# Kernel tuning notes

Measured on AMD Instinct MI355X. Metric: run time of the kernel, lower is better.

## Reference

```python
import jax, jax.numpy as jnp
import numpy as np

B, T, E, H = 2, 2048, 1024, 16


def setup_inputs() -> dict:
    key = jax.random.key(0)
    ks = jax.random.split(key, 8)
    # VarianceScaling(1.0) ~ truncated normal with stddev ~ sqrt(1/fan_in)
    std = 1.0 / np.sqrt(E)
    x = jax.random.normal(ks[0], (B, T, E), dtype=jnp.float32)
    y = jax.random.normal(ks[1], (B, T, E), dtype=jnp.float32)
    # causal mask [1, 1, T, T]
    mask = jnp.tril(jnp.ones((T, T), dtype=jnp.float32))[None, None]
    Wq = jax.random.normal(ks[2], (E, E), dtype=jnp.float32) * std
    Wk = jax.random.normal(ks[3], (E, E), dtype=jnp.float32) * std
    Wv = jax.random.normal(ks[4], (E, E), dtype=jnp.float32) * std
    Wo = jax.random.normal(ks[5], (E, E), dtype=jnp.float32) * std
    bq = jnp.zeros((E,), jnp.float32)
    bk = jnp.zeros((E,), jnp.float32)
    bv = jnp.zeros((E,), jnp.float32)
    bo = jnp.zeros((E,), jnp.float32)
    return {"x": x, "y": y, "mask": mask, "Wq": Wq, "bq": bq,
            "Wk": Wk, "bk": bk, "Wv": Wv, "bv": bv, "Wo": Wo, "bo": bo,
            "num_heads": H}


def reference(x, y, mask, Wq, bq, Wk, bk, Wv, bv, Wo, bo, num_heads):
    Bx, Tq, Emb = x.shape
    Tkv = y.shape[1]
    d = Emb // num_heads
    q = (x @ Wq + bq).reshape(Bx, Tq, num_heads, d)
    k = (y @ Wk + bk).reshape(Bx, Tkv, num_heads, d)
    v = (y @ Wv + bv).reshape(Bx, Tkv, num_heads, d)
    scale = 1.0 / np.sqrt(d).astype(np.float32)
    att = scale * jnp.einsum('bthd,bThd->bhtT', q, k)  # [B,H,Tq,Tkv]
    att = att * mask - 1e10 * (1.0 - mask)
    att = jax.nn.softmax(att, axis=-1)
    out = jnp.einsum('bhtT,bThd->bthd', att, v).reshape(Bx, Tq, Emb)
    return out @ Wo + bo
```

## Files before the change

### kernel.cpp

```cpp
#include <hip/hip_runtime.h>
#include <stdint.h>

#define BB 2
#define TT 2048
#define EE 1024
#define HH 16
#define DD 64
#define MM (BB*TT)

typedef unsigned short u16;
typedef __attribute__((ext_vector_type(4))) float f32x4;
typedef __attribute__((ext_vector_type(8))) __bf16 bf16x8;
typedef __attribute__((ext_vector_type(8))) u16 u16x8;
typedef __attribute__((ext_vector_type(4))) u16 u16x4;

union FragU { u16x8 u; bf16x8 b; };
union BfU { __bf16 h; u16 u; };

__device__ __forceinline__ u16 f2bf(float f) {
  uint32_t u = __float_as_uint(f);
  u += 0x7fffu + ((u >> 16) & 1u);
  return (u16)(u >> 16);
}

__device__ __forceinline__ void gload16(const u16* __restrict__ g, u16* l) {
  __builtin_amdgcn_global_load_lds((const __attribute__((address_space(1))) void*)g,
                                   (__attribute__((address_space(3))) void*)l, 16, 0, 0);
}

__global__ __launch_bounds__(256) void prep(const float* __restrict__ x, const float* __restrict__ y,
                                            const float* __restrict__ Wq, const float* __restrict__ Wk,
                                            const float* __restrict__ Wv, const float* __restrict__ Wo,
                                            u16* __restrict__ xb, u16* __restrict__ yb,
                                            u16* __restrict__ Wqt, u16* __restrict__ Wkvt,
                                            u16* __restrict__ Wot) {
  __shared__ alignas(16) float tile[64][65];
  int bi = blockIdx.x, t = threadIdx.x;
  if (bi < 4096) {
    const float* src = (bi < 2048) ? x : y;
    u16* dst = (bi < 2048) ? xb : yb;
    int i = (bi & 2047) * 256 + t;
    const f32x4* s4 = (const f32x4*)src;
    f32x4 a = s4[2*i], b = s4[2*i+1];
    u16x8 o;
    o[0]=f2bf(a[0]); o[1]=f2bf(a[1]); o[2]=f2bf(a[2]); o[3]=f2bf(a[3]);
    o[4]=f2bf(b[0]); o[5]=f2bf(b[1]); o[6]=f2bf(b[2]); o[7]=f2bf(b[3]);
    ((u16x8*)dst)[i] = o;
    return;
  }
  int wi = bi - 4096;
  int z = wi >> 8;
  const float* W; u16* Tp;
  switch (z) {
    case 0: W = Wq; Tp = Wqt; break;
    case 1: W = Wk; Tp = Wkvt; break;
    case 2: W = Wv; Tp = Wkvt + (size_t)1024*EE; break;
    default: W = Wo; Tp = Wot; break;
  }
  int r8 = wi & 255;
  int n0 = (r8 & 15) * 64, k0 = (r8 >> 4) * 64;
#pragma unroll
  for (int i = 0; i < 16; ++i) {
    int idx = i*256 + t; int r = idx >> 6, c = idx & 63;
    tile[r][c] = W[(size_t)(k0 + r) * EE + n0 + c];
  }
  __syncthreads();
#pragma unroll
  for (int i = 0; i < 16; ++i) {
    int idx = i*256 + t; int rn = idx >> 6, ck = idx & 63;
    Tp[(size_t)(n0 + rn) * EE + k0 + ck] = f2bf(tile[ck][rn]);
  }
}

template <int BM, int EPI>
__device__ __forceinline__ void gemm_body(const u16* __restrict__ A, const u16* __restrict__ Bt,
                                          const float* __restrict__ bias, void* __restrict__ Cout,
                                          int N, int K, float oscale, int bm, int bn,
                                          u16 (*As)[64], u16 (*Bs)[64]) {
  constexpr int MI = BM / 32;
  const int t = threadIdx.x;
  const int lane = t & 63, w = t >> 6;
  const int wr = w >> 1, wc = w & 1;
  const int g = lane >> 4, cl = lane & 15;

  f32x4 acc[MI][4] = {};

  const u16* Ag = A + (size_t)(bm * BM) * K;
  const u16* Bg = Bt + (size_t)(bn * 128) * K;

  const int rl = lane >> 3;
  const int sw = ((lane & 7) ^ rl) * 8;

  const int nk = K / 64;
  for (int kt = 0; kt < nk; ++kt) {
    const int k0 = kt * 64;
    __syncthreads();
#pragma unroll
    for (int j = 0; j < MI; ++j) {
      int ca = w * MI + j;
      gload16(Ag + (size_t)(ca*8 + rl) * K + k0 + sw, &As[ca*8][0]);
    }
#pragma unroll
    for (int j = 0; j < 4; ++j) {
      int cb = w * 4 + j;
      gload16(Bg + (size_t)(cb*8 + rl) * K + k0 + sw, &Bs[cb*8][0]);
    }
    __syncthreads();
#pragma unroll
    for (int ks = 0; ks < 2; ++ks) {
      FragU af[MI], bfr[4];
#pragma unroll
      for (int mi = 0; mi < MI; ++mi) {
        int row = wr*(BM/2) + mi*16 + cl;
        af[mi].u = *(const u16x8*)&As[row][((ks*4 + g) ^ (row & 7)) * 8];
      }
#pragma unroll
      for (int nj = 0; nj < 4; ++nj) {
        int row = wc*64 + nj*16 + cl;
        bfr[nj].u = *(const u16x8*)&Bs[row][((ks*4 + g) ^ (row & 7)) * 8];
      }
#pragma unroll
      for (int mi = 0; mi < MI; ++mi)
#pragma unroll
        for (int nj = 0; nj < 4; ++nj)
          acc[mi][nj] = __builtin_amdgcn_mfma_f32_16x16x32_bf16(af[mi].b, bfr[nj].b, acc[mi][nj], 0, 0, 0);
    }
  }

  const int cbase = bn*128 + wc*64 + cl;
  float bv[4];
#pragma unroll
  for (int nj = 0; nj < 4; ++nj) bv[nj] = bias[cbase + nj*16];
#pragma unroll
  for (int mi = 0; mi < MI; ++mi) {
    int row0 = bm*BM + wr*(BM/2) + mi*16 + (g << 2);
    if (EPI == 2) {
      int bb = row0 >> 11;
      int tt = row0 & 2047;
      int tb64 = tt & ~63;
      int w6 = tt & 63;
      int p = ((w6 >> 5) << 5) | (((w6 >> 2) & 3) << 3) | (((w6 >> 4) & 1) << 2);
#pragma unroll
      for (int nj = 0; nj < 4; ++nj) {
        int cc = cbase + nj*16;
        int hh = cc >> 6, dd = cc & 63;
        u16x4 v;
#pragma unroll
        for (int i = 0; i < 4; ++i) v[i] = f2bf(acc[mi][nj][i] + bv[nj]);
        *(u16x4*)((u16*)Cout + ((size_t)((bb*HH + hh)*DD + dd))*2048 + tb64 + p) = v;
      }
    } else {
#pragma unroll
      for (int i = 0; i < 4; ++i) {
        if (EPI == 1) {
          float* Cp = (float*)Cout + (size_t)(row0 + i) * N + cbase;
#pragma unroll
          for (int nj = 0; nj < 4; ++nj)
            Cp[nj*16] = (acc[mi][nj][i] + bv[nj]) * oscale;
        } else {
          u16* Cp = (u16*)Cout + (size_t)(row0 + i) * N + cbase;
#pragma unroll
          for (int nj = 0; nj < 4; ++nj)
            Cp[nj*16] = f2bf((acc[mi][nj][i] + bv[nj]) * oscale);
        }
      }
    }
  }
}

__global__ __launch_bounds__(256) void gemm_qkv(const u16* __restrict__ xb, const u16* __restrict__ yb,
                                                const u16* __restrict__ Wqt, const u16* __restrict__ Wkvt,
                                                const float* __restrict__ bq, const float* __restrict__ bk,
                                                const float* __restrict__ bv,
                                                u16* __restrict__ Qb, u16* __restrict__ Kb,
                                                u16* __restrict__ Vtb, float c1) {
  __shared__ alignas(16) u16 As[128][64];
  __shared__ alignas(16) u16 Bs[128][64];
  const int i = blockIdx.x;
  const int l = (i & 7) * 96 + (i >> 3);
  const int bm = l / 24, bx = l % 24;
  if (bx < 8)
    gemm_body<128, 0>(xb, Wqt, bq, Qb, 1024, EE, c1, bm, bx, As, Bs);
  else if (bx < 16)
    gemm_body<128, 0>(yb, Wkvt, bk, Kb, 1024, EE, 1.0f, bm, bx - 8, As, Bs);
  else
    gemm_body<128, 2>(yb, Wkvt + (size_t)1024*EE, bv, Vtb, 1024, EE, 1.0f, bm, bx - 16, As, Bs);
}

__global__ __launch_bounds__(256) void gemm_o(const u16* __restrict__ Atb, const u16* __restrict__ Wot,
                                              const float* __restrict__ bo, float* __restrict__ out) {
  __shared__ alignas(16) u16 As[64][64];
  __shared__ alignas(16) u16 Bs[128][64];
  const int i = blockIdx.x;
  const int l = (i & 7) * 64 + (i >> 3);
  const int bm = l / 8, bn = l % 8;
  gemm_body<64, 1>(Atb, Wot, bo, out, 1024, EE, 1.0f, bm, bn, As, Bs);
}

__global__ __launch_bounds__(512, 4) void attn(const u16* __restrict__ Q, const u16* __restrict__ Kb,
                                               const u16* __restrict__ Vt, u16* __restrict__ O) {
  const int i0 = blockIdx.x;
  const int qq = i0 >> 8, a = (i0 >> 5) & 7, bh = i0 & 31;
  int qt;
  switch (qq) {
    case 0:  qt = 31 - a; break;
    case 1:  qt = 16 + a; break;
    case 2:  qt = 15 - a; break;
    default: qt = a;      break;
  }
  const int b = bh >> 4, h = bh & 15;

  const int t = threadIdx.x, lane = t & 63, w = t >> 6;
  const int ws_ = w & 3;
  const int hi = w >> 2;
  const int g = lane >> 4, c = lane & 15;
  __shared__ alignas(16) u16 Ks[2][64][72];
  __shared__ alignas(16) u16 Vs[2][64][72];

  const int qw0 = qt * 64 + ws_ * 16;

  FragU qf[2];
  const u16* Qbase = Q + ((size_t)(b*TT) + qw0) * EE + h*DD;
#pragma unroll
  for (int ks = 0; ks < 2; ++ks)
    qf[ks].u = *(const u16x8*)(Qbase + (size_t)c * EE + ks*32 + g*8);

  f32x4 oacc[4] = {};
  float l_part = 0.f;
  float m_run = -1e30f;

  const u16* Kbase = Kb + (size_t)(b*TT) * 1024 + h*DD;
  const u16* Vtbase = Vt + (size_t)(b*HH + h) * DD * 2048;

  const int nkv = qt + 1;
  const int npair = (nkv + 1) >> 1;

  const int srow = t >> 3;
  const int scol = (t & 7) * 8;

  u16x8 rk[2], rv[2];
  rk[0] = *(const u16x8*)(Kbase + (size_t)srow * 1024 + scol);
  rv[0] = *(const u16x8*)(Vtbase + (size_t)srow * 2048 + scol);
  if (1 < nkv) {
    rk[1] = *(const u16x8*)(Kbase + (size_t)(64 + srow) * 1024 + scol);
    rv[1] = *(const u16x8*)(Vtbase + (size_t)srow * 2048 + 64 + scol);
  }

  for (int jj = 0; jj < npair; ++jj) {
    const int j0 = 2*jj;
    __syncthreads();
    *(u16x8*)&Ks[0][srow][scol] = rk[0];
    *(u16x8*)&Vs[0][srow][scol] = rv[0];
    if (j0 + 1 < nkv) {
      *(u16x8*)&Ks[1][srow][scol] = rk[1];
      *(u16x8*)&Vs[1][srow][scol] = rv[1];
    }
    __syncthreads();
    if (jj + 1 < npair) {
      const int jn = 2*(jj + 1);
      rk[0] = *(const u16x8*)(Kbase + (size_t)(jn*64 + srow) * 1024 + scol);
      rv[0] = *(const u16x8*)(Vtbase + (size_t)srow * 2048 + jn*64 + scol);
      if (jn + 1 < nkv) {
        rk[1] = *(const u16x8*)(Kbase + (size_t)((jn+1)*64 + srow) * 1024 + scol);
        rv[1] = *(const u16x8*)(Vtbase + (size_t)srow * 2048 + (jn+1)*64 + scol);
      }
    }
    const int j = j0 + hi;
    const int kv0 = j * 64;
    if (j >= nkv || kv0 > qw0 + 15) continue;

    f32x4 s[4] = {};
    __builtin_amdgcn_s_setprio(1);
#pragma unroll
    for (int ks = 0; ks < 2; ++ks) {
      const int kc = ks*32 + g*8;
      FragU kf[4];
#pragma unroll
      for (int nj = 0; nj < 4; ++nj)
        kf[nj].u = *(const u16x8*)&Ks[hi][nj*16 + c][kc];
#pragma unroll
      for (int nj = 0; nj < 4; ++nj)
        s[nj] = __builtin_amdgcn_mfma_f32_16x16x32_bf16(kf[nj].b, qf[ks].b, s[nj], 0, 0, 0);
    }
    __builtin_amdgcn_s_setprio(0);

    const bool full = (kv0 + 63 <= qw0);
    float vmax;
    if (full) {
      float m0 = fmaxf(fmaxf(s[0][0], s[0][1]), fmaxf(s[0][2], s[0][3]));
      float m1 = fmaxf(fmaxf(s[1][0], s[1][1]), fmaxf(s[1][2], s[1][3]));
      float m2 = fmaxf(fmaxf(s[2][0], s[2][1]), fmaxf(s[2][2], s[2][3]));
      float m3 = fmaxf(fmaxf(s[3][0], s[3][1]), fmaxf(s[3][2], s[3][3]));
      vmax = fmaxf(fmaxf(m0, m1), fmaxf(m2, m3));
    } else {
      const int q = qw0 + c;
      vmax = -1e30f;
#pragma unroll
      for (int nj = 0; nj < 4; ++nj)
#pragma unroll
        for (int r = 0; r < 4; ++r) {
          float xv = s[nj][r];
          if (kv0 + nj*16 + 4*g + r > q) xv = -1e30f;
          s[nj][r] = xv;
          vmax = fmaxf(vmax, xv);
        }
    }

    if (__any(vmax > m_run + 8.f)) {
      float vm = vmax;
      vm = fmaxf(vm, __shfl_xor(vm, 1));
      vm = fmaxf(vm, __shfl_xor(vm, 2));
      vm = fmaxf(vm, __shfl_xor(vm, 4));
      vm = fmaxf(vm, __shfl_xor(vm, 8));
      vm = fmaxf(vm, __shfl_xor(vm, 16));
      vm = fmaxf(vm, __shfl_xor(vm, 32));
      float f = exp2f(m_run - vm);
      l_part *= f;
#pragma unroll
      for (int dj = 0; dj < 4; ++dj)
#pragma unroll
        for (int i = 0; i < 4; ++i) oacc[dj][i] *= f;
      m_run = vm;
    }

    FragU pa[2];
    float psum = 0.f;
#pragma unroll
    for (int nj = 0; nj < 4; ++nj)
#pragma unroll
      for (int r = 0; r < 4; ++r) {
        float p = exp2f(s[nj][r] - m_run);
        psum += p;
        BfU cv; cv.h = (__bf16)p;
        pa[nj >> 1].u[(nj & 1) * 4 + r] = cv.u;
      }
    l_part += psum;

    __builtin_amdgcn_s_setprio(1);
#pragma unroll
    for (int ks = 0; ks < 2; ++ks) {
#pragma unroll
      for (int dj = 0; dj < 4; ++dj) {
        FragU vf;
        vf.u = *(const u16x8*)&Vs[hi][dj*16 + c][ks*32 + g*8];
        oacc[dj] = __builtin_amdgcn_mfma_f32_16x16x32_bf16(pa[ks].b, vf.b, oacc[dj], 0, 0, 0);
      }
    }
    __builtin_amdgcn_s_setprio(0);
  }

  __syncthreads();
  l_part += __shfl_xor(l_part, 16);
  l_part += __shfl_xor(l_part, 32);

  float* mO = (float*)&Ks[0][0][0];
  float* mL = (float*)&Vs[0][0][0];

  if (hi) {
#pragma unroll
    for (int i = 0; i < 4; ++i) {
      int row = 4*g + i;
#pragma unroll
      for (int dj = 0; dj < 4; ++dj)
        mO[((size_t)(ws_*16 + row))*66 + dj*16 + c] = oacc[dj][i];
    }
    if (lane < 16) mL[ws_*16 + lane] = l_part;
    if (lane == 0) mL[64 + ws_] = m_run;
  }
  __syncthreads();
  if (!hi) {
    float m1 = mL[64 + ws_];
    float l1 = mL[ws_*16 + c];
    float mN = fmaxf(m_run, m1);
    float f0 = exp2f(m_run - mN);
    float f1 = exp2f(m1 - mN);
    float lm = l_part * f0 + l1 * f1;
    u16* Ob = O + ((size_t)(b*TT) + qw0) * EE + h*DD;
#pragma unroll
    for (int i = 0; i < 4; ++i) {
      int row = 4*g + i;
      float li = __shfl(lm, row);
      float inv = 1.f / li;
#pragma unroll
      for (int dj = 0; dj < 4; ++dj) {
        float o1 = mO[((size_t)(ws_*16 + row))*66 + dj*16 + c];
        Ob[(size_t)row * EE + dj*16 + c] = f2bf((oacc[dj][i] * f0 + o1 * f1) * inv);
      }
    }
  }
}

extern "C" void kernel_launch(void* const* d_in, const int* in_sizes, int n_in,
                              void* d_out, int out_size, void* d_ws, size_t ws_size,
                              hipStream_t stream) {
  const float* x  = (const float*)d_in[0];
  const float* y  = (const float*)d_in[1];
  const float* Wq = (const float*)d_in[3];
  const float* bq = (const float*)d_in[4];
  const float* Wk = (const float*)d_in[5];
  const float* bk = (const float*)d_in[6];
  const float* Wv = (const float*)d_in[7];
  const float* bv = (const float*)d_in[8];
  const float* Wo = (const float*)d_in[9];
  const float* bo = (const float*)d_in[10];

  if (ws_size < (size_t)58720256) return;

  char* ws = (char*)d_ws;
  u16* Wqt  = (u16*)(ws + 0);
  u16* Wkvt = (u16*)(ws + 2097152);
  u16* Wot  = (u16*)(ws + 6291456);
  u16* Qb   = (u16*)(ws + 8388608);
  u16* Kb   = (u16*)(ws + 16777216);
  u16* Vtb  = (u16*)(ws + 25165824);
  u16* Atb  = (u16*)(ws + 33554432);
  u16* xb   = (u16*)(ws + 41943040);
  u16* yb   = (u16*)(ws + 50331648);

  const float c1 = 0.125f * 1.44269504088896340736f;

  prep<<<5120, 256, 0, stream>>>(x, y, Wq, Wk, Wv, Wo, xb, yb, Wqt, Wkvt, Wot);
  gemm_qkv<<<768, 256, 0, stream>>>(xb, yb, Wqt, Wkvt, bq, bk, bv, Qb, Kb, Vtb, c1);
  attn<<<1024, 512, 0, stream>>>(Qb, Kb, Vtb, Atb);
  gemm_o<<<512, 256, 0, stream>>>(Atb, Wot, bo, (float*)d_out);
}
```

Before: 118.5 us.

## Split long causal attention tiles across blocks with separate merge kernel

Replaces the in-block two-wavegroup KV split with a split-KV scheme. Query tiles in the upper half of the sequence are split into two blocks that each cover half of the KV range and write unnormalized partial outputs and softmax stats to workspace. A new merge kernel combines the two partials. Shorter tiles run whole in 256-thread blocks. The aim is better load balance and occupancy, at the cost of an extra launch and fp32 partial traffic. The partial buffer reuses the xb/yb workspace region.

```diff
diff --git a/kernel.cpp b/kernel.cpp
--- a/kernel.cpp
+++ b/kernel.cpp
@@ -16,6 +16,8 @@
 
 union FragU { u16x8 u; bf16x8 b; };
 union BfU { __bf16 h; u16 u; };
+
+#define PSLOT 4224
 
 __device__ __forceinline__ u16 f2bf(float f) {
   uint32_t u = __float_as_uint(f);
@@ -197,27 +199,32 @@
   gemm_body<64, 1>(Atb, Wot, bo, out, 1024, EE, 1.0f, bm, bn, As, Bs);
 }
 
-__global__ __launch_bounds__(512, 4) void attn(const u16* __restrict__ Q, const u16* __restrict__ Kb,
-                                               const u16* __restrict__ Vt, u16* __restrict__ O) {
+__global__ __launch_bounds__(256, 6) void attn(const u16* __restrict__ Q, const u16* __restrict__ Kb,
+                                               const u16* __restrict__ Vt, u16* __restrict__ O,
+                                               float* __restrict__ Pp) {
   const int i0 = blockIdx.x;
-  const int qq = i0 >> 8, a = (i0 >> 5) & 7, bh = i0 & 31;
-  int qt;
-  switch (qq) {
-    case 0:  qt = 31 - a; break;
-    case 1:  qt = 16 + a; break;
-    case 2:  qt = 15 - a; break;
-    default: qt = a;      break;
+  const int bh = i0 & 31, u = i0 >> 5;
+  int qt, c0, c1;
+  bool partial;
+  if (u < 32) {
+    qt = 31 - (u >> 1);
+    const int nkv = qt + 1, mid = (nkv + 1) >> 1;
+    c0 = (u & 1) ? mid : 0;
+    c1 = (u & 1) ? nkv : mid;
+    partial = true;
+  } else {
+    qt = 47 - u;
+    c0 = 0; c1 = qt + 1;
+    partial = false;
   }
   const int b = bh >> 4, h = bh & 15;
 
   const int t = threadIdx.x, lane = t & 63, w = t >> 6;
-  const int ws_ = w & 3;
-  const int hi = w >> 2;
   const int g = lane >> 4, c = lane & 15;
-  __shared__ alignas(16) u16 Ks[2][64][72];
-  __shared__ alignas(16) u16 Vs[2][64][72];
-
-  const int qw0 = qt * 64 + ws_ * 16;
+  __shared__ alignas(16) u16 Ks[64][72];
+  __shared__ alignas(16) u16 Vs[64][72];
+
+  const int qw0 = qt * 64 + w * 16;
 
   FragU qf[2];
   const u16* Qbase = Q + ((size_t)(b*TT) + qw0) * EE + h*DD;
@@ -232,42 +239,34 @@
   const u16* Kbase = Kb + (size_t)(b*TT) * 1024 + h*DD;
   const u16* Vtbase = Vt + (size_t)(b*HH + h) * DD * 2048;
 
-  const int nkv = qt + 1;
-  const int npair = (nkv + 1) >> 1;
-
-  const int srow = t >> 3;
+  const int srow0 = t >> 3;
+  const int srow1 = 32 + srow0;
   const int scol = (t & 7) * 8;
 
   u16x8 rk[2], rv[2];
-  rk[0] = *(const u16x8*)(Kbase + (size_t)srow * 1024 + scol);
-  rv[0] = *(const u16x8*)(Vtbase + (size_t)srow * 2048 + scol);
-  if (1 < nkv) {
-    rk[1] = *(const u16x8*)(Kbase + (size_t)(64 + srow) * 1024 + scol);
-    rv[1] = *(const u16x8*)(Vtbase + (size_t)srow * 2048 + 64 + scol);
-  }
-
-  for (int jj = 0; jj < npair; ++jj) {
-    const int j0 = 2*jj;
+  {
+    const int kv0 = c0 * 64;
+    rk[0] = *(const u16x8*)(Kbase + (size_t)(kv0 + srow0) * 1024 + scol);
+    rk[1] = *(const u16x8*)(Kbase + (size_t)(kv0 + srow1) * 1024 + scol);
+    rv[0] = *(const u16x8*)(Vtbase + (size_t)srow0 * 2048 + kv0 + scol);
+    rv[1] = *(const u16x8*)(Vtbase + (size_t)srow1 * 2048 + kv0 + scol);
+  }
+
+  for (int j = c0; j < c1; ++j) {
+    const int kv0 = j * 64;
     __syncthreads();
-    *(u16x8*)&Ks[0][srow][scol] = rk[0];
-    *(u16x8*)&Vs[0][srow][scol] = rv[0];
-    if (j0 + 1 < nkv) {
-      *(u16x8*)&Ks[1][srow][scol] = rk[1];
-      *(u16x8*)&Vs[1][srow][scol] = rv[1];
-    }
+    *(u16x8*)&Ks[srow0][scol] = rk[0];
+    *(u16x8*)&Ks[srow1][scol] = rk[1];
+    *(u16x8*)&Vs[srow0][scol] = rv[0];
+    *(u16x8*)&Vs[srow1][scol] = rv[1];
     __syncthreads();
-    if (jj + 1 < npair) {
-      const int jn = 2*(jj + 1);
-      rk[0] = *(const u16x8*)(Kbase + (size_t)(jn*64 + srow) * 1024 + scol);
-      rv[0] = *(const u16x8*)(Vtbase + (size_t)srow * 2048 + jn*64 + scol);
-      if (jn + 1 < nkv) {
-        rk[1] = *(const u16x8*)(Kbase + (size_t)((jn+1)*64 + srow) * 1024 + scol);
-        rv[1] = *(const u16x8*)(Vtbase + (size_t)srow * 2048 + (jn+1)*64 + scol);
-      }
-    }
-    const int j = j0 + hi;
-    const int kv0 = j * 64;
-    if (j >= nkv || kv0 > qw0 + 15) continue;
+    if (j + 1 < c1) {
+      const int kv1 = kv0 + 64;
+      rk[0] = *(const u16x8*)(Kbase + (size_t)(kv1 + srow0) * 1024 + scol);
+      rk[1] = *(const u16x8*)(Kbase + (size_t)(kv1 + srow1) * 1024 + scol);
+      rv[0] = *(const u16x8*)(Vtbase + (size_t)srow0 * 2048 + kv1 + scol);
+      rv[1] = *(const u16x8*)(Vtbase + (size_t)srow1 * 2048 + kv1 + scol);
+    }
 
     f32x4 s[4] = {};
     __builtin_amdgcn_s_setprio(1);
@@ -277,7 +276,7 @@
       FragU kf[4];
 #pragma unroll
       for (int nj = 0; nj < 4; ++nj)
-        kf[nj].u = *(const u16x8*)&Ks[hi][nj*16 + c][kc];
+        kf[nj].u = *(const u16x8*)&Ks[nj*16 + c][kc];
 #pragma unroll
       for (int nj = 0; nj < 4; ++nj)
         s[nj] = __builtin_amdgcn_mfma_f32_16x16x32_bf16(kf[nj].b, qf[ks].b, s[nj], 0, 0, 0);
@@ -342,51 +341,67 @@
 #pragma unroll
       for (int dj = 0; dj < 4; ++dj) {
         FragU vf;
-        vf.u = *(const u16x8*)&Vs[hi][dj*16 + c][ks*32 + g*8];
+        vf.u = *(const u16x8*)&Vs[dj*16 + c][ks*32 + g*8];
         oacc[dj] = __builtin_amdgcn_mfma_f32_16x16x32_bf16(pa[ks].b, vf.b, oacc[dj], 0, 0, 0);
       }
     }
     __builtin_amdgcn_s_setprio(0);
   }
 
-  __syncthreads();
   l_part += __shfl_xor(l_part, 16);
   l_part += __shfl_xor(l_part, 32);
 
-  float* mO = (float*)&Ks[0][0][0];
-  float* mL = (float*)&Vs[0][0][0];
-
-  if (hi) {
+  if (partial) {
+    float* po = Pp + (size_t)((((bh << 4) | (qt - 16)) << 1) | (u & 1)) * PSLOT;
+#pragma unroll
+    for (int i = 0; i < 4; ++i) {
+      int row = w*16 + 4*g + i;
+#pragma unroll
+      for (int dj = 0; dj < 4; ++dj)
+        po[row*64 + dj*16 + c] = oacc[dj][i];
+    }
+    if (lane < 16) {
+      po[4096 + w*16 + lane] = l_part;
+      po[4160 + w*16 + lane] = m_run;
+    }
+  } else {
+    u16* Ob = O + ((size_t)(b*TT) + qw0) * EE + h*DD;
 #pragma unroll
     for (int i = 0; i < 4; ++i) {
       int row = 4*g + i;
+      float li = __shfl(l_part, 4*g + i);
+      float inv = 1.f / li;
 #pragma unroll
       for (int dj = 0; dj < 4; ++dj)
-        mO[((size_t)(ws_*16 + row))*66 + dj*16 + c] = oacc[dj][i];
-    }
-    if (lane < 16) mL[ws_*16 + lane] = l_part;
-    if (lane == 0) mL[64 + ws_] = m_run;
-  }
-  __syncthreads();
-  if (!hi) {
-    float m1 = mL[64 + ws_];
-    float l1 = mL[ws_*16 + c];
-    float mN = fmaxf(m_run, m1);
-    float f0 = exp2f(m_run - mN);
-    float f1 = exp2f(m1 - mN);
-    float lm = l_part * f0 + l1 * f1;
-    u16* Ob = O + ((size_t)(b*TT) + qw0) * EE + h*DD;
-#pragma unroll
-    for (int i = 0; i < 4; ++i) {
-      int row = 4*g + i;
-      float li = __shfl(lm, row);
-      float inv = 1.f / li;
-#pragma unroll
-      for (int dj = 0; dj < 4; ++dj) {
-        float o1 = mO[((size_t)(ws_*16 + row))*66 + dj*16 + c];
-        Ob[(size_t)row * EE + dj*16 + c] = f2bf((oacc[dj][i] * f0 + o1 * f1) * inv);
-      }
-    }
+        Ob[(size_t)row * EE + dj*16 + c] = f2bf(oacc[dj][i] * inv);
+    }
+  }
+}
+
+__global__ __launch_bounds__(256) void attn_merge(const float* __restrict__ Pp, u16* __restrict__ O) {
+  const int bi = blockIdx.x;
+  const int bh = bi >> 4, qt = (bi & 15) + 16;
+  const int b = bh >> 4, h = bh & 15;
+  const int t = threadIdx.x;
+  const int r = t >> 2, cg = (t & 3) * 16;
+
+  const float* p0 = Pp + (size_t)(bi << 1) * PSLOT;
+  const float* p1 = p0 + PSLOT;
+  float l0 = p0[4096 + r], m0 = p0[4160 + r];
+  float l1 = p1[4096 + r], m1 = p1[4160 + r];
+  float mN = fmaxf(m0, m1);
+  float f0 = exp2f(m0 - mN), f1 = exp2f(m1 - mN);
+  float inv = 1.f / (f0 * l0 + f1 * l1);
+
+  u16* Ob = O + ((size_t)(b*TT) + qt*64 + r) * EE + h*DD + cg;
+#pragma unroll
+  for (int j = 0; j < 4; ++j) {
+    f32x4 o0 = *(const f32x4*)&p0[r*64 + cg + j*4];
+    f32x4 o1 = *(const f32x4*)&p1[r*64 + cg + j*4];
+    u16x4 v;
+#pragma unroll
+    for (int e = 0; e < 4; ++e) v[e] = f2bf((o0[e]*f0 + o1[e]*f1) * inv);
+    *(u16x4*)(Ob + j*4) = v;
   }
 }
 
@@ -404,7 +419,7 @@
   const float* Wo = (const float*)d_in[9];
   const float* bo = (const float*)d_in[10];
 
-  if (ws_size < (size_t)58720256) return;
+  if (ws_size < (size_t)62914560) return;
 
   char* ws = (char*)d_ws;
   u16* Wqt  = (u16*)(ws + 0);
@@ -416,11 +431,13 @@
   u16* Atb  = (u16*)(ws + 33554432);
   u16* xb   = (u16*)(ws + 41943040);
   u16* yb   = (u16*)(ws + 50331648);
+  float* Pp = (float*)(ws + 41943040);
 
   const float c1 = 0.125f * 1.44269504088896340736f;
 
   prep<<<5120, 256, 0, stream>>>(x, y, Wq, Wk, Wv, Wo, xb, yb, Wqt, Wkvt, Wot);
   gemm_qkv<<<768, 256, 0, stream>>>(xb, yb, Wqt, Wkvt, bq, bk, bv, Qb, Kb, Vtb, c1);
-  attn<<<1024, 512, 0, stream>>>(Qb, Kb, Vtb, Atb);
+  attn<<<1536, 256, 0, stream>>>(Qb, Kb, Vtb, Atb, Pp);
+  attn_merge<<<512, 256, 0, stream>>>(Pp, Atb);
   gemm_o<<<512, 256, 0, stream>>>(Atb, Wot, bo, (float*)d_out);
 }
```

Result: slower. 129.1 us (+8.9%).
